# Performance work log

Hardware: AMD Instinct MI355X
Metric: run time of the kernel (lower is better)

## Reference

```python
import jax, jax.numpy as jnp
import numpy as np

B, N, C = 4, 1370, 1024
H, DH = 16, C // 16
N_ROPE = 1369  # patch tokens covered by RoPE (prefix=1 CLS token)


def _rotate_half(x):
    x1, x2 = jnp.split(x, 2, axis=-1)
    return jnp.concatenate([-x2, x1], axis=-1)


def _rope_apply(x, sin, cos):
    return x * cos + _rotate_half(x) * sin


def setup_inputs() -> dict:
    key = jax.random.key(0)
    ks = jax.random.split(key, 7)
    return {
        "x": jax.random.normal(ks[0], (B, N, C), dtype=jnp.float32),
        "sin": jax.random.normal(ks[1], (N_ROPE, DH), dtype=jnp.float32),
        "cos": jax.random.normal(ks[2], (N_ROPE, DH), dtype=jnp.float32),
        "w_qkv": jax.random.normal(ks[3], (C, 3 * C), dtype=jnp.float32) * (C ** -0.5),
        "b_qkv": jax.random.normal(ks[4], (3 * C,), dtype=jnp.float32) * 0.02,
        "w_proj": jax.random.normal(ks[5], (C, C), dtype=jnp.float32) * (C ** -0.5),
        "b_proj": jax.random.normal(ks[6], (C,), dtype=jnp.float32) * 0.02,
    }


def reference(x, sin, cos, w_qkv, b_qkv, w_proj, b_proj):
    b, n, c = x.shape
    # QKV projection -> [3, B, H, N, DH]
    qkv = (x @ w_qkv + b_qkv).reshape(b, n, 3, H, DH).transpose(2, 0, 3, 1, 4)
    q, k, v = qkv[0], qkv[1], qkv[2]
    # RoPE on the last N_ROPE tokens (prefix tokens, e.g. CLS, left untouched)
    prefix = n - sin.shape[-2]
    q = jnp.concatenate([q[:, :, :prefix, :], _rope_apply(q[:, :, prefix:, :], sin, cos)], axis=-2)
    k = jnp.concatenate([k[:, :, :prefix, :], _rope_apply(k[:, :, prefix:, :], sin, cos)], axis=-2)
    # Full attention
    scale = 1.0 / jnp.sqrt(jnp.asarray(DH, dtype=x.dtype))
    attn = jnp.einsum('bhqd,bhkd->bhqk', q, k) * scale
    attn = jax.nn.softmax(attn, axis=-1)
    out = jnp.einsum('bhqk,bhkd->bhqd', attn, v)
    out = out.transpose(0, 2, 1, 3).reshape(b, n, c)
    return out @ w_proj + b_proj
```

## Files before the change

kernel.cpp:

```cpp
#include <hip/hip_runtime.h>
#include <hip/hip_bf16.h>

#define B_ 4
#define N_ 1370
#define C_ 1024
#define H_ 16
#define DH_ 64
#define NR_ 1369
#define M_ (B_*N_)
#define VTS_ 1408
#define ALS 64
#define PLS 72

#define QSCALE 0.1803368801111f

typedef _Float16 f16x8  __attribute__((ext_vector_type(8)));
typedef __bf16   bf16x8 __attribute__((ext_vector_type(8)));
typedef float    f32x4  __attribute__((ext_vector_type(4)));

__device__ __forceinline__ f16x8 ld_frag_h(const unsigned short* p) {
    uint4 u = *(const uint4*)p;
    return __builtin_bit_cast(f16x8, u);
}
__device__ __forceinline__ bf16x8 ld_frag_b(const unsigned short* p) {
    uint4 u = *(const uint4*)p;
    return __builtin_bit_cast(bf16x8, u);
}
__device__ __forceinline__ unsigned short f2h(float f) {
    _Float16 h = (_Float16)f;
    return __builtin_bit_cast(unsigned short, h);
}
__device__ __forceinline__ unsigned short f2bf(float f) {
    __hip_bfloat16 h = __float2bfloat16(f);
    return __builtin_bit_cast(unsigned short, h);
}
__device__ __forceinline__ bf16x8 ones_bf() {
    uint4 u = make_uint4(0x3F803F80u, 0x3F803F80u, 0x3F803F80u, 0x3F803F80u);
    return __builtin_bit_cast(bf16x8, u);
}

__device__ __forceinline__ void load_lds16(const unsigned short* g, unsigned short* l) {
    __builtin_amdgcn_global_load_lds(
        (const __attribute__((address_space(1))) unsigned int*)g,
        (__attribute__((address_space(3))) unsigned int*)l,
        16, 0, 0);
}

#define XBLK 5480
#define WQBLK 768
#define WPBLK 256
__global__ __launch_bounds__(256)
void prep_k(const float* __restrict__ x, unsigned short* __restrict__ xo,
            const float* __restrict__ wq, unsigned short* __restrict__ wqt,
            const float* __restrict__ wp, unsigned short* __restrict__ wpt)
{
    __shared__ unsigned short Th[64][68];
    int bid = blockIdx.x;
    if (bid < XBLK) {
        const int i = bid * 256 + threadIdx.x;
        float4 v = ((const float4*)x)[i];
        ushort4 h;
        h.x = f2h(v.x); h.y = f2h(v.y); h.z = f2h(v.z); h.w = f2h(v.w);
        ((ushort4*)xo)[i] = h;
        return;
    }
    bid -= XBLK;
    const float* w; unsigned short* wt; int Ncol, nb;
    if (bid < WQBLK) { w = wq; wt = wqt; Ncol = 3072; nb = 48; }
    else { bid -= WQBLK; w = wp; wt = wpt; Ncol = 1024; nb = 16; }
    const int tid = threadIdx.x, tx = tid & 15, ty = tid >> 4;
    const int n0 = (bid % nb) * 64, k0 = (bid / nb) * 64;
    #pragma unroll
    for (int i = 0; i < 4; ++i) {
        const int k = ty + i * 16;
        float4 v = *(const float4*)&w[(size_t)(k0 + k) * Ncol + n0 + tx * 4];
        Th[k][tx*4+0] = f2h(v.x); Th[k][tx*4+1] = f2h(v.y);
        Th[k][tx*4+2] = f2h(v.z); Th[k][tx*4+3] = f2h(v.w);
    }
    __syncthreads();
    #pragma unroll
    for (int i = 0; i < 4; ++i) {
        const int n = ty + i * 16;
        ushort4 o;
        o.x = Th[tx*4+0][n]; o.y = Th[tx*4+1][n]; o.z = Th[tx*4+2][n]; o.w = Th[tx*4+3][n];
        *(ushort4*)&wt[(size_t)(n0 + n) * 1024 + k0 + tx * 4] = o;
    }
}

__global__ __launch_bounds__(256)
void transpose_v_k(const unsigned short* __restrict__ v, unsigned short* __restrict__ vt) {
    __shared__ unsigned short Th[64][68];
    const int tid = threadIdx.x, tx = tid & 15, ty = tid >> 4;
    const int bh = blockIdx.y, t0 = blockIdx.x * 64;
    const unsigned short* vp = v + (size_t)bh * N_ * DH_;
    unsigned short* vtp = vt + (size_t)bh * DH_ * VTS_;
    #pragma unroll
    for (int i = 0; i < 4; ++i) {
        const int tok = ty + i * 16;
        const int gtok = t0 + tok;
        ushort4 val;
        if (gtok < N_) val = *(const ushort4*)&vp[(size_t)gtok * DH_ + tx * 4];
        else { val.x = 0; val.y = 0; val.z = 0; val.w = 0; }
        Th[tok][tx*4+0] = val.x; Th[tok][tx*4+1] = val.y;
        Th[tok][tx*4+2] = val.z; Th[tok][tx*4+3] = val.w;
    }
    __syncthreads();
    #pragma unroll
    for (int i = 0; i < 4; ++i) {
        const int d = ty + i * 16;
        ushort4 o;
        o.x = Th[tx*4+0][d]; o.y = Th[tx*4+1][d]; o.z = Th[tx*4+2][d]; o.w = Th[tx*4+3][d];
        *(ushort4*)&vtp[(size_t)d * VTS_ + t0 + tx * 4] = o;
    }
}

template<int MODE, int NBLK, int GRID>
__global__ __launch_bounds__(512, 4)
void gemm8(const unsigned short* __restrict__ A, const unsigned short* __restrict__ Bt,
           const float* __restrict__ bias, float* __restrict__ out,
           unsigned short* __restrict__ qb, unsigned short* __restrict__ kb,
           unsigned short* __restrict__ vb,
           const float* __restrict__ sinp, const float* __restrict__ cosp)
{
    __shared__ __align__(16) unsigned short A_s[2][192 * 64];
    __shared__ __align__(16) unsigned short B_s[2][128 * 64];

    const int tid = threadIdx.x;
    const int wave = tid >> 6, lane = tid & 63;
    const int quad = lane >> 4, l16 = lane & 15;

    const int id  = blockIdx.x;
    const int lid = (id & 7) * (GRID / 8) + (id >> 3);
    const int mblk = lid / NBLK, nblk = lid - mblk * NBLK;
    const int m0 = mblk * 192, n0 = nblk * 128;

    const int mwave = (wave >> 1) * 48;
    const int nwave = (wave & 1) * 64;

    const int srow = lane >> 3;
    const int gseg = (lane & 7) ^ srow;

    f32x4 acc[3][4] = {};

    auto stage = [&](int kc, int buf) {
        const int kof = kc * 64;
        #pragma unroll
        for (int i = 0; i < 3; ++i) {
            const int rbase = wave * 24 + i * 8;
            int arow = m0 + rbase + srow;
            if (arow > M_ - 1) arow = M_ - 1;
            load_lds16(A + (size_t)arow * 1024 + kof + gseg * 8, &A_s[buf][rbase * 64]);
        }
        #pragma unroll
        for (int i = 0; i < 2; ++i) {
            const int rbase = wave * 16 + i * 8;
            const int brow = n0 + rbase + srow;
            load_lds16(Bt + (size_t)brow * 1024 + kof + gseg * 8, &B_s[buf][rbase * 64]);
        }
    };

    stage(0, 0);

    for (int kc = 0; kc < 16; ++kc) {
        const int cur = kc & 1;
        __syncthreads();
        if (kc + 1 < 16) stage(kc + 1, cur ^ 1);

        #pragma unroll
        for (int kh = 0; kh < 2; ++kh) {
            const int soff = (((kh * 4 + quad) ^ (l16 & 7)) << 3);
            f16x8 a[3], b[4];
            #pragma unroll
            for (int t = 0; t < 3; ++t)
                a[t] = ld_frag_h(&A_s[cur][(mwave + t * 16 + l16) * 64 + soff]);
            #pragma unroll
            for (int t = 0; t < 4; ++t)
                b[t] = ld_frag_h(&B_s[cur][(nwave + t * 16 + l16) * 64 + soff]);
            #pragma unroll
            for (int i = 0; i < 3; ++i)
                #pragma unroll
                for (int j = 0; j < 4; ++j)
                    acc[i][j] = __builtin_amdgcn_mfma_f32_16x16x32_f16(a[i], b[j], acc[i][j], 0, 0, 0);
        }
    }

    if (MODE == 0) {
        #pragma unroll
        for (int i = 0; i < 3; ++i) {
            #pragma unroll
            for (int r = 0; r < 4; ++r) {
                const int gm = m0 + mwave + i * 16 + quad * 4 + r;
                if (gm >= M_) continue;
                #pragma unroll
                for (int j = 0; j < 4; ++j) {
                    const int gn = n0 + nwave + j * 16 + l16;
                    out[(size_t)gm * 1024 + gn] = acc[i][j][r] + bias[gn];
                }
            }
        }
    } else {
        const int nbase = n0 + nwave;
        const int part = nbase >> 10;
        const int h = (nbase & 1023) >> 6;
        #pragma unroll
        for (int i = 0; i < 3; ++i) {
            #pragma unroll
            for (int r = 0; r < 4; ++r) {
                const int gm = m0 + mwave + i * 16 + quad * 4 + r;
                if (gm >= M_) continue;
                const int b = gm / N_;
                const int tok = gm - b * N_;

                float val[4];
                #pragma unroll
                for (int j = 0; j < 4; ++j)
                    val[j] = acc[i][j][r] + bias[nbase + j * 16 + l16];

                if (part < 2 && tok >= 1) {
                    const float* sp = sinp + (size_t)(tok - 1) * DH_;
                    const float* cp = cosp + (size_t)(tok - 1) * DH_;
                    const float s0 = sp[l16],      s1 = sp[16 + l16];
                    const float s2 = sp[32 + l16], s3 = sp[48 + l16];
                    const float c0 = cp[l16],      c1 = cp[16 + l16];
                    const float c2 = cp[32 + l16], c3 = cp[48 + l16];
                    const float n0v = fmaf(val[0], c0, -val[2] * s0);
                    const float n1v = fmaf(val[1], c1, -val[3] * s1);
                    const float n2v = fmaf(val[2], c2,  val[0] * s2);
                    const float n3v = fmaf(val[3], c3,  val[1] * s3);
                    val[0] = n0v; val[1] = n1v; val[2] = n2v; val[3] = n3v;
                }

                const int bh = b * H_ + h;
                #pragma unroll
                for (int j = 0; j < 4; ++j) {
                    const int d = j * 16 + l16;
                    if (part == 0)      qb[((size_t)bh * N_ + tok) * DH_ + d] = f2h(val[j] * QSCALE);
                    else if (part == 1) kb[((size_t)bh * N_ + tok) * DH_ + d] = f2h(val[j]);
                    else                vb[((size_t)bh * N_ + tok) * DH_ + d] = f2bf(val[j]);
                }
            }
        }
    }
}

__global__ __launch_bounds__(512, 6)
void attn_k(const unsigned short* __restrict__ q, const unsigned short* __restrict__ k,
            const unsigned short* __restrict__ vt, unsigned short* __restrict__ out)
{
    __shared__ __align__(16) unsigned short Ks[2][64 * ALS];
    __shared__ __align__(16) unsigned short Vs[2][64 * ALS];
    __shared__ __align__(16) unsigned short Ps[8 * 16 * PLS];

    const int tid  = threadIdx.x;
    const int wave = tid >> 6, lane = tid & 63;
    const int quad = lane >> 4, l16 = lane & 15;
    const int srow = lane >> 3;
    const int gseg = (lane & 7) ^ srow;

    const int id  = blockIdx.x;
    const int lid = (id & 7) * 88 + (id >> 3);
    const int bh  = lid / 11;
    const int q0  = (lid - bh * 11) * 128;

    const unsigned short* qp  = q  + (size_t)bh * N_ * DH_;
    const unsigned short* kp  = k  + (size_t)bh * N_ * DH_;
    const unsigned short* vtp = vt + (size_t)bh * DH_ * VTS_;

    f16x8 qf[2];
    {
        int qrow = q0 + wave * 16 + l16;
        if (qrow > N_ - 1) qrow = N_ - 1;
        qf[0] = ld_frag_h(qp + (size_t)qrow * DH_ + quad * 8);
        qf[1] = ld_frag_h(qp + (size_t)qrow * DH_ + 32 + quad * 8);
    }

    const bf16x8 onesv = ones_bf();
    f32x4 O[4] = {};
    f32x4 L = {};

    unsigned short* Pw = Ps + wave * 16 * PLS;
    const int so0 = ((quad)     ^ (l16 & 7)) << 3;
    const int so1 = ((4 + quad) ^ (l16 & 7)) << 3;

    auto stage = [&](int ch, int buf) {
        const int k0 = ch * 64;
        const int rbase = wave * 8;
        int krow = k0 + rbase + srow;
        if (krow > N_ - 1) krow = N_ - 1;
        load_lds16(kp + (size_t)krow * DH_ + gseg * 8, &Ks[buf][rbase * ALS]);
        load_lds16(vtp + (size_t)(rbase + srow) * VTS_ + k0 + gseg * 8, &Vs[buf][rbase * ALS]);
    };

    stage(0, 0);

    for (int ch = 0; ch < 22; ++ch) {
        const int k0 = ch * 64;
        const int cur = ch & 1;
        __syncthreads();
        if (ch + 1 < 22) stage(ch + 1, 1 - cur);

        f16x8 kf[4][2];
        #pragma unroll
        for (int t = 0; t < 4; ++t) {
            kf[t][0] = ld_frag_h(&Ks[cur][(t * 16 + l16) * ALS + so0]);
            kf[t][1] = ld_frag_h(&Ks[cur][(t * 16 + l16) * ALS + so1]);
        }
        f32x4 S[4];
        #pragma unroll
        for (int t = 0; t < 4; ++t) {
            f32x4 z = {};
            z = __builtin_amdgcn_mfma_f32_16x16x32_f16(qf[0], kf[t][0], z, 0, 0, 0);
            z = __builtin_amdgcn_mfma_f32_16x16x32_f16(qf[1], kf[t][1], z, 0, 0, 0);
            S[t] = z;
        }
        if (k0 + 64 > N_) {
            #pragma unroll
            for (int t = 0; t < 4; ++t) {
                if (k0 + t * 16 + l16 >= N_) {
                    S[t][0] = -1e30f; S[t][1] = -1e30f;
                    S[t][2] = -1e30f; S[t][3] = -1e30f;
                }
            }
        }

        #pragma unroll
        for (int t = 0; t < 4; ++t) {
            #pragma unroll
            for (int r = 0; r < 4; ++r) {
                const float p = __builtin_amdgcn_exp2f(S[t][r]);
                Pw[(quad * 4 + r) * PLS + t * 16 + l16] = f2bf(p);
            }
        }
        __builtin_amdgcn_wave_barrier();

        bf16x8 pf[2];
        pf[0] = ld_frag_b(&Pw[l16 * PLS + quad * 8]);
        pf[1] = ld_frag_b(&Pw[l16 * PLS + 32 + quad * 8]);

        bf16x8 vf[4][2];
        #pragma unroll
        for (int dt = 0; dt < 4; ++dt) {
            vf[dt][0] = ld_frag_b(&Vs[cur][(dt * 16 + l16) * ALS + so0]);
            vf[dt][1] = ld_frag_b(&Vs[cur][(dt * 16 + l16) * ALS + so1]);
        }
        L = __builtin_amdgcn_mfma_f32_16x16x32_bf16(pf[0], onesv, L, 0, 0, 0);
        L = __builtin_amdgcn_mfma_f32_16x16x32_bf16(pf[1], onesv, L, 0, 0, 0);
        #pragma unroll
        for (int dt = 0; dt < 4; ++dt) {
            O[dt] = __builtin_amdgcn_mfma_f32_16x16x32_bf16(pf[0], vf[dt][0], O[dt], 0, 0, 0);
            O[dt] = __builtin_amdgcn_mfma_f32_16x16x32_bf16(pf[1], vf[dt][1], O[dt], 0, 0, 0);
        }
    }

    const int b = bh >> 4, h = bh & 15;
    #pragma unroll
    for (int r = 0; r < 4; ++r) {
        const int qi = q0 + wave * 16 + quad * 4 + r;
        if (qi < N_) {
            const float inv = 1.0f / L[r];
            unsigned short* op = out + ((size_t)(b * N_ + qi)) * C_ + h * DH_ + l16;
            #pragma unroll
            for (int dt = 0; dt < 4; ++dt) op[dt * 16] = f2h(O[dt][r] * inv);
        }
    }
}

extern "C" void kernel_launch(void* const* d_in, const int* in_sizes, int n_in,
                              void* d_out, int out_size, void* d_ws, size_t ws_size,
                              hipStream_t stream) {
    const float* x      = (const float*)d_in[0];
    const float* sinp   = (const float*)d_in[1];
    const float* cosp   = (const float*)d_in[2];
    const float* w_qkv  = (const float*)d_in[3];
    const float* b_qkv  = (const float*)d_in[4];
    const float* w_proj = (const float*)d_in[5];
    const float* b_proj = (const float*)d_in[6];
    float* out = (float*)d_out;

    unsigned short* p = (unsigned short*)d_ws;
    const size_t xsz  = (size_t)M_ * C_;
    const size_t wqsz = (size_t)3 * C_ * C_;
    const size_t wpsz = (size_t)C_ * C_;
    const size_t hsz  = (size_t)B_ * H_ * N_ * DH_;
    const size_t vtsz = (size_t)B_ * H_ * DH_ * VTS_;
    unsigned short* x_h   = p;            p += xsz;
    unsigned short* wq_t  = p;            p += wqsz;
    unsigned short* wp_t  = p;            p += wpsz;
    unsigned short* q     = p;            p += hsz;
    unsigned short* k     = p;            p += hsz;
    unsigned short* vt    = p;            p += vtsz;
    unsigned short* attnb = p;            p += xsz;
    unsigned short* vb    = attnb;

    prep_k<<<dim3(XBLK + WQBLK + WPBLK), 256, 0, stream>>>(
        x, x_h, w_qkv, wq_t, w_proj, wp_t);

    gemm8<1, 24, 696><<<dim3(696), 512, 0, stream>>>(
        x_h, wq_t, b_qkv, nullptr, q, k, vb, sinp, cosp);

    transpose_v_k<<<dim3(VTS_ / 64, B_ * H_), 256, 0, stream>>>(vb, vt);

    attn_k<<<dim3(11 * B_ * H_), 512, 0, stream>>>(q, k, vt, attnb);

    gemm8<0, 8, 232><<<dim3(232), 512, 0, stream>>>(
        attnb, wp_t, b_proj, out, nullptr, nullptr, nullptr, nullptr, nullptr);
}
```

Baseline: 232.9 us.

## Make QKV GEMM persistent with atomic tile counter for dynamic scheduling

The QKV projection GEMM now launches 512 persistent blocks. Each block repeatedly claims a 192x128 output tile from a global atomic counter until all tiles are done, replacing the fixed one-tile-per-block grid of 696 blocks with its swizzled tile order. The counter is reset inside the preceding prep kernel. The aim is to balance the uneven tail wave and to cut block launch overhead. The cost is an atomic plus an extra barrier per tile, and tiles are now claimed in plain linear order, so the earlier L2-friendly swizzle is lost.

```diff
diff --git a/kernel.cpp b/kernel.cpp
--- a/kernel.cpp
+++ b/kernel.cpp
@@ -52,11 +52,13 @@
 __global__ __launch_bounds__(256)
 void prep_k(const float* __restrict__ x, unsigned short* __restrict__ xo,
             const float* __restrict__ wq, unsigned short* __restrict__ wqt,
-            const float* __restrict__ wp, unsigned short* __restrict__ wpt)
+            const float* __restrict__ wp, unsigned short* __restrict__ wpt,
+            unsigned* __restrict__ qctr)
 {
     __shared__ unsigned short Th[64][68];
     int bid = blockIdx.x;
     if (bid < XBLK) {
+        if (bid == 0 && threadIdx.x == 0) *qctr = 0u;
         const int i = bid * 256 + threadIdx.x;
         float4 v = ((const float4*)x)[i];
         ushort4 h;
@@ -120,27 +122,26 @@
            const float* __restrict__ bias, float* __restrict__ out,
            unsigned short* __restrict__ qb, unsigned short* __restrict__ kb,
            unsigned short* __restrict__ vb,
-           const float* __restrict__ sinp, const float* __restrict__ cosp)
+           const float* __restrict__ sinp, const float* __restrict__ cosp,
+           unsigned* __restrict__ ctr)
 {
+    constexpr int NT = ((M_ + 191) / 192) * NBLK;
+
     __shared__ __align__(16) unsigned short A_s[2][192 * 64];
     __shared__ __align__(16) unsigned short B_s[2][128 * 64];
+    __shared__ int tileS;
 
     const int tid = threadIdx.x;
     const int wave = tid >> 6, lane = tid & 63;
     const int quad = lane >> 4, l16 = lane & 15;
 
-    const int id  = blockIdx.x;
-    const int lid = (id & 7) * (GRID / 8) + (id >> 3);
-    const int mblk = lid / NBLK, nblk = lid - mblk * NBLK;
-    const int m0 = mblk * 192, n0 = nblk * 128;
-
     const int mwave = (wave >> 1) * 48;
     const int nwave = (wave & 1) * 64;
 
     const int srow = lane >> 3;
     const int gseg = (lane & 7) ^ srow;
 
-    f32x4 acc[3][4] = {};
+    int m0 = 0, n0 = 0;
 
     auto stage = [&](int kc, int buf) {
         const int kof = kc * 64;
@@ -159,84 +160,102 @@
         }
     };
 
-    stage(0, 0);
-
-    for (int kc = 0; kc < 16; ++kc) {
-        const int cur = kc & 1;
-        __syncthreads();
-        if (kc + 1 < 16) stage(kc + 1, cur ^ 1);
-
-        #pragma unroll
-        for (int kh = 0; kh < 2; ++kh) {
-            const int soff = (((kh * 4 + quad) ^ (l16 & 7)) << 3);
-            f16x8 a[3], b[4];
-            #pragma unroll
-            for (int t = 0; t < 3; ++t)
-                a[t] = ld_frag_h(&A_s[cur][(mwave + t * 16 + l16) * 64 + soff]);
-            #pragma unroll
-            for (int t = 0; t < 4; ++t)
-                b[t] = ld_frag_h(&B_s[cur][(nwave + t * 16 + l16) * 64 + soff]);
-            #pragma unroll
-            for (int i = 0; i < 3; ++i)
+    for (;;) {
+        int tile;
+        if (MODE == 1) {
+            if (tid == 0) tileS = (int)atomicAdd(ctr, 1u);
+            __syncthreads();
+            tile = tileS;
+            if (tile >= NT) break;
+        } else {
+            const int id  = blockIdx.x;
+            tile = (id & 7) * (GRID / 8) + (id >> 3);
+        }
+        const int mblk = tile / NBLK, nblk = tile - mblk * NBLK;
+        m0 = mblk * 192; n0 = nblk * 128;
+
+        f32x4 acc[3][4] = {};
+
+        stage(0, 0);
+
+        for (int kc = 0; kc < 16; ++kc) {
+            const int cur = kc & 1;
+            __syncthreads();
+            if (kc + 1 < 16) stage(kc + 1, cur ^ 1);
+
+            #pragma unroll
+            for (int kh = 0; kh < 2; ++kh) {
+                const int soff = (((kh * 4 + quad) ^ (l16 & 7)) << 3);
+                f16x8 a[3], b[4];
                 #pragma unroll
-                for (int j = 0; j < 4; ++j)
-                    acc[i][j] = __builtin_amdgcn_mfma_f32_16x16x32_f16(a[i], b[j], acc[i][j], 0, 0, 0);
-        }
-    }
-
-    if (MODE == 0) {
-        #pragma unroll
-        for (int i = 0; i < 3; ++i) {
-            #pragma unroll
-            for (int r = 0; r < 4; ++r) {
-                const int gm = m0 + mwave + i * 16 + quad * 4 + r;
-                if (gm >= M_) continue;
+                for (int t = 0; t < 3; ++t)
+                    a[t] = ld_frag_h(&A_s[cur][(mwave + t * 16 + l16) * 64 + soff]);
                 #pragma unroll
-                for (int j = 0; j < 4; ++j) {
-                    const int gn = n0 + nwave + j * 16 + l16;
-                    out[(size_t)gm * 1024 + gn] = acc[i][j][r] + bias[gn];
+                for (int t = 0; t < 4; ++t)
+                    b[t] = ld_frag_h(&B_s[cur][(nwave + t * 16 + l16) * 64 + soff]);
+                #pragma unroll
+                for (int i = 0; i < 3; ++i)
+                    #pragma unroll
+                    for (int j = 0; j < 4; ++j)
+                        acc[i][j] = __builtin_amdgcn_mfma_f32_16x16x32_f16(a[i], b[j], acc[i][j], 0, 0, 0);
+            }
+        }
+
+        if (MODE == 0) {
+            #pragma unroll
+            for (int i = 0; i < 3; ++i) {
+                #pragma unroll
+                for (int r = 0; r < 4; ++r) {
+                    const int gm = m0 + mwave + i * 16 + quad * 4 + r;
+                    if (gm >= M_) continue;
+                    #pragma unroll
+                    for (int j = 0; j < 4; ++j) {
+                        const int gn = n0 + nwave + j * 16 + l16;
+                        out[(size_t)gm * 1024 + gn] = acc[i][j][r] + bias[gn];
+                    }
                 }
             }
-        }
-    } else {
-        const int nbase = n0 + nwave;
-        const int part = nbase >> 10;
-        const int h = (nbase & 1023) >> 6;
-        #pragma unroll
-        for (int i = 0; i < 3; ++i) {
-            #pragma unroll
-            for (int r = 0; r < 4; ++r) {
-                const int gm = m0 + mwave + i * 16 + quad * 4 + r;
-                if (gm >= M_) continue;
-                const int b = gm / N_;
-                const int tok = gm - b * N_;
-
-                float val[4];
+            break;
+        } else {
+            const int nbase = n0 + nwave;
+            const int part = nbase >> 10;
+            const int h = (nbase & 1023) >> 6;
+            #pragma unroll
+            for (int i = 0; i < 3; ++i) {
                 #pragma unroll
-                for (int j = 0; j < 4; ++j)
-                    val[j] = acc[i][j][r] + bias[nbase + j * 16 + l16];
-
-                if (part < 2 && tok >= 1) {
-                    const float* sp = sinp + (size_t)(tok - 1) * DH_;
-                    const float* cp = cosp + (size_t)(tok - 1) * DH_;
-                    const float s0 = sp[l16],      s1 = sp[16 + l16];
-                    const float s2 = sp[32 + l16], s3 = sp[48 + l16];
-                    const float c0 = cp[l16],      c1 = cp[16 + l16];
-                    const float c2 = cp[32 + l16], c3 = cp[48 + l16];
-                    const float n0v = fmaf(val[0], c0, -val[2] * s0);
-                    const float n1v = fmaf(val[1], c1, -val[3] * s1);
-                    const float n2v = fmaf(val[2], c2,  val[0] * s2);
-                    const float n3v = fmaf(val[3], c3,  val[1] * s3);
-                    val[0] = n0v; val[1] = n1v; val[2] = n2v; val[3] = n3v;
-                }
-
-                const int bh = b * H_ + h;
-                #pragma unroll
-                for (int j = 0; j < 4; ++j) {
-                    const int d = j * 16 + l16;
-                    if (part == 0)      qb[((size_t)bh * N_ + tok) * DH_ + d] = f2h(val[j] * QSCALE);
-                    else if (part == 1) kb[((size_t)bh * N_ + tok) * DH_ + d] = f2h(val[j]);
-                    else                vb[((size_t)bh * N_ + tok) * DH_ + d] = f2bf(val[j]);
+                for (int r = 0; r < 4; ++r) {
+                    const int gm = m0 + mwave + i * 16 + quad * 4 + r;
+                    if (gm >= M_) continue;
+                    const int b = gm / N_;
+                    const int tok = gm - b * N_;
+
+                    float val[4];
+                    #pragma unroll
+                    for (int j = 0; j < 4; ++j)
+                        val[j] = acc[i][j][r] + bias[nbase + j * 16 + l16];
+
+                    if (part < 2 && tok >= 1) {
+                        const float* sp = sinp + (size_t)(tok - 1) * DH_;
+                        const float* cp = cosp + (size_t)(tok - 1) * DH_;
+                        const float s0 = sp[l16],      s1 = sp[16 + l16];
+                        const float s2 = sp[32 + l16], s3 = sp[48 + l16];
+                        const float c0 = cp[l16],      c1 = cp[16 + l16];
+                        const float c2 = cp[32 + l16], c3 = cp[48 + l16];
+                        const float n0v = fmaf(val[0], c0, -val[2] * s0);
+                        const float n1v = fmaf(val[1], c1, -val[3] * s1);
+                        const float n2v = fmaf(val[2], c2,  val[0] * s2);
+                        const float n3v = fmaf(val[3], c3,  val[1] * s3);
+                        val[0] = n0v; val[1] = n1v; val[2] = n2v; val[3] = n3v;
+                    }
+
+                    const int bh = b * H_ + h;
+                    #pragma unroll
+                    for (int j = 0; j < 4; ++j) {
+                        const int d = j * 16 + l16;
+                        if (part == 0)      qb[((size_t)bh * N_ + tok) * DH_ + d] = f2h(val[j] * QSCALE);
+                        else if (part == 1) kb[((size_t)bh * N_ + tok) * DH_ + d] = f2h(val[j]);
+                        else                vb[((size_t)bh * N_ + tok) * DH_ + d] = f2bf(val[j]);
+                    }
                 }
             }
         }
@@ -390,18 +409,19 @@
     unsigned short* k     = p;            p += hsz;
     unsigned short* vt    = p;            p += vtsz;
     unsigned short* attnb = p;            p += xsz;
+    unsigned*       qctr  = (unsigned*)p; p += 2;
     unsigned short* vb    = attnb;
 
     prep_k<<<dim3(XBLK + WQBLK + WPBLK), 256, 0, stream>>>(
-        x, x_h, w_qkv, wq_t, w_proj, wp_t);
-
-    gemm8<1, 24, 696><<<dim3(696), 512, 0, stream>>>(
-        x_h, wq_t, b_qkv, nullptr, q, k, vb, sinp, cosp);
+        x, x_h, w_qkv, wq_t, w_proj, wp_t, qctr);
+
+    gemm8<1, 24, 512><<<dim3(512), 512, 0, stream>>>(
+        x_h, wq_t, b_qkv, nullptr, q, k, vb, sinp, cosp, qctr);
 
     transpose_v_k<<<dim3(VTS_ / 64, B_ * H_), 256, 0, stream>>>(vb, vt);
 
     attn_k<<<dim3(11 * B_ * H_), 512, 0, stream>>>(q, k, vt, attnb);
 
     gemm8<0, 8, 232><<<dim3(232), 512, 0, stream>>>(
-        attnb, wp_t, b_proj, out, nullptr, nullptr, nullptr, nullptr, nullptr);
-}
+        attnb, wp_t, b_proj, out, nullptr, nullptr, nullptr, nullptr, nullptr, nullptr);
+}
```

Measured after the change: 249.6 us. +7.2%, slower.
